# Optimization experiments

Measured on AMD Instinct MI355X. Metric: run time of the kernel, lower is better.

The kernel has to match this reference:

```python
import jax, jax.numpy as jnp
import numpy as np

B, T, D = 2, 2048, 2048
H, HD = 16, 128
ROPE_BASE = 10000.0
EPS = 1e-6


def setup_inputs() -> dict:
    key = jax.random.key(0)
    ks = jax.random.split(key, 5)
    s = 1.0 / np.sqrt(D)
    return {
        "x": jax.random.normal(ks[0], (B, T, D), dtype=jnp.float32),
        "Wq": jax.random.normal(ks[1], (H * HD, D), dtype=jnp.float32) * s,
        "Wk": jax.random.normal(ks[2], (H * HD, D), dtype=jnp.float32) * s,
        "Wv": jax.random.normal(ks[3], (H * HD, D), dtype=jnp.float32) * s,
        "Wo": jax.random.normal(ks[4], (D, H * HD), dtype=jnp.float32) * s,
        "q_norm_w": jnp.ones((HD,), dtype=jnp.float32),
        "k_norm_w": jnp.ones((HD,), dtype=jnp.float32),
    }


def _rms_norm(x, w):
    # RMSNorm over last dim, no centering (LLaMA/Qwen style)
    norm = jnp.sqrt(jnp.mean(jnp.square(x), axis=-1, keepdims=True) + EPS)
    return x / norm * w


def _rope_interleaved(x):
    # x: (B, T, H, HD); GPT-NeoX interleaved style, sequential positions
    dim = HD // 2
    freqs = jnp.exp(-jnp.arange(0, dim, dtype=jnp.float32) * jnp.log(ROPE_BASE) / dim)
    angles = jnp.arange(T, dtype=jnp.float32)[:, None] * freqs[None, :]  # (T, dim)
    cos = jnp.cos(angles)[None, :, None, :]  # (1, T, 1, dim)
    sin = jnp.sin(angles)[None, :, None, :]
    x_even = x[..., ::2]
    x_odd = x[..., 1::2]
    r_even = x_even * cos - x_odd * sin
    r_odd = x_even * sin + x_odd * cos
    return jnp.stack([r_even, r_odd], axis=-1).reshape(x.shape)


def reference(x, Wq, Wk, Wv, Wo, q_norm_w, k_norm_w):
    # QKV projections (weights stored [out, in], per llm_linear einsum)
    q = jnp.einsum("btd,od->bto", x, Wq).reshape(B, T, H, HD)
    k = jnp.einsum("btd,od->bto", x, Wk).reshape(B, T, H, HD)
    v = jnp.einsum("btd,od->bto", x, Wv).reshape(B, T, H, HD)
    # per-head QK RMSNorm
    q = _rms_norm(q, q_norm_w)
    k = _rms_norm(k, k_norm_w)
    # rotary embeddings
    q = _rope_interleaved(q)
    k = _rope_interleaved(k)
    # causal scaled dot-product attention
    scale = 1.0 / jnp.sqrt(jnp.asarray(HD, dtype=x.dtype))
    scores = jnp.einsum("bthd,bshd->bhts", q, k) * scale  # (B, H, T, T)
    causal = jnp.tril(jnp.ones((T, T), dtype=bool))
    scores = jnp.where(causal[None, None, :, :], scores, jnp.asarray(-1e30, dtype=scores.dtype))
    probs = jax.nn.softmax(scores, axis=-1)
    ctx = jnp.einsum("bhts,bshd->bthd", probs, v).reshape(B, T, H * HD)
    # output projection
    return jnp.einsum("bto,do->btd", ctx, Wo)
```

## Files before the change

### kernel.cpp

```cpp
#include <hip/hip_runtime.h>
#include <cstdint>
#include <cstddef>

#define B_ 2
#define T_ 2048
#define D_ 2048
#define H_ 16
#define HD_ 128
#define EPS_ 1e-6f
#define QSCALE_ 0.08838834764831845f
#define KVSTRIDE_ (H_ * HD_)

typedef unsigned short u16;
typedef short s16x8 __attribute__((ext_vector_type(8)));
typedef float f32x4 __attribute__((ext_vector_type(4)));

__device__ __forceinline__ float bf2f(u16 h) {
  union { unsigned int u; float f; } v;
  v.u = ((unsigned int)h) << 16;
  return v.f;
}
__device__ __forceinline__ u16 f2bf(float f) {
  union { float f; unsigned int u; } v;
  v.f = f;
  unsigned int r = v.u + 0x7FFFu + ((v.u >> 16) & 1u);
  return (u16)(r >> 16);
}

__device__ __forceinline__ void gload16(const void* g, void* l) {
  __builtin_amdgcn_global_load_lds(
      (const __attribute__((address_space(1))) unsigned int*)g,
      (__attribute__((address_space(3))) unsigned int*)l, 16, 0, 0);
}

__global__ void cvt_f32_bf16(const float* __restrict__ in, u16* __restrict__ out, int n4) {
  int i = blockIdx.x * blockDim.x + threadIdx.x;
  if (i < n4) {
    float4 v = ((const float4*)in)[i];
    ((ushort4*)out)[i] = make_ushort4(f2bf(v.x), f2bf(v.y), f2bf(v.z), f2bf(v.w));
  }
}

template <int OUT_BF16>
__global__ __launch_bounds__(256, 2) void gemm_btn(const u16* __restrict__ A,
                                                   const u16* __restrict__ Bm,
                                                   void* __restrict__ Cout,
                                                   int M, int N, int K) {
  __shared__ u16 As[2 * 128 * 32];
  __shared__ u16 Bs[2 * 128 * 32];
  const int tid = threadIdx.x;
  const int w = tid >> 6, lane = tid & 63, quad = lane >> 4, c = lane & 15;
  const int wm = w & 1, wn = w >> 1;
  const int m0 = blockIdx.y * 128, n0 = blockIdx.x * 128;

  f32x4 acc[4][4];
#pragma unroll
  for (int i = 0; i < 4; ++i)
#pragma unroll
    for (int j = 0; j < 4; ++j) acc[i][j] = (f32x4){0.f, 0.f, 0.f, 0.f};

  for (int k0 = 0; k0 < K; k0 += 64) {
    __syncthreads();
#pragma unroll
    for (int i = 0; i < 4; ++i) {
      int chunk = (w * 4 + i) * 64 + lane;
      int kc = chunk >> 9;
      int within = chunk & 511;
      int row = within >> 2, cc = within & 3;
      gload16(A + (size_t)(m0 + row) * K + k0 + kc * 32 + cc * 8, (void*)(As + chunk * 8));
      gload16(Bm + (size_t)(n0 + row) * K + k0 + kc * 32 + cc * 8, (void*)(Bs + chunk * 8));
    }
    __syncthreads();
#pragma unroll
    for (int kc = 0; kc < 2; ++kc) {
      s16x8 af[4], bf[4];
#pragma unroll
      for (int mi = 0; mi < 4; ++mi)
        af[mi] = *(const s16x8*)(As + kc * 4096 + (wm * 64 + mi * 16 + c) * 32 + quad * 8);
#pragma unroll
      for (int ni = 0; ni < 4; ++ni)
        bf[ni] = *(const s16x8*)(Bs + kc * 4096 + (wn * 64 + ni * 16 + c) * 32 + quad * 8);
#pragma unroll
      for (int mi = 0; mi < 4; ++mi)
#pragma unroll
        for (int ni = 0; ni < 4; ++ni)
          acc[mi][ni] = __builtin_amdgcn_mfma_f32_16x16x32_bf16(af[mi], bf[ni], acc[mi][ni], 0, 0, 0);
    }
  }

#pragma unroll
  for (int mi = 0; mi < 4; ++mi)
#pragma unroll
    for (int ni = 0; ni < 4; ++ni)
#pragma unroll
      for (int r = 0; r < 4; ++r) {
        int row = m0 + wm * 64 + mi * 16 + quad * 4 + r;
        int col = n0 + wn * 64 + ni * 16 + c;
        float v = acc[mi][ni][r];
        if (OUT_BF16)
          ((u16*)Cout)[(size_t)row * N + col] = f2bf(v);
        else
          ((float*)Cout)[(size_t)row * N + col] = v;
      }
}

__global__ void rmsnorm_rope(u16* __restrict__ x, const float* __restrict__ nw, float outscale) {
  const int tid = threadIdx.x;
  const int w = tid >> 6, lane = tid & 63;
  const int vec = blockIdx.x * 4 + w;
  const int t = (vec >> 4) & (T_ - 1);
  u16* base = x + (size_t)vec * HD_;
  unsigned int pk = *(const unsigned int*)(base + lane * 2);
  float e = bf2f((u16)(pk & 0xFFFFu));
  float o = bf2f((u16)(pk >> 16));
  float ss = e * e + o * o;
#pragma unroll
  for (int off = 1; off < 64; off <<= 1) ss += __shfl_xor(ss, off, 64);
  float rn = rsqrtf(ss * (1.0f / HD_) + EPS_);
  float we = nw[lane * 2], wo = nw[lane * 2 + 1];
  e = e * rn * we;
  o = o * rn * wo;
  float freq = expf(-(float)lane * (9.210340371976184f / 64.0f));
  float ang = (float)t * freq;
  float sn, cs;
  sincosf(ang, &sn, &cs);
  float re = (e * cs - o * sn) * outscale;
  float ro = (e * sn + o * cs) * outscale;
  *(unsigned int*)(base + lane * 2) = ((unsigned int)f2bf(ro) << 16) | (unsigned int)f2bf(re);
}

__global__ __launch_bounds__(256, 2) void attn_fwd(const u16* __restrict__ Q,
                                                   const u16* __restrict__ Kg,
                                                   const u16* __restrict__ Vt,
                                                   u16* __restrict__ O) {
  __shared__ u16 Ks[64 * 136];
  __shared__ u16 Vts[128 * 72];
  __shared__ u16 Ps[64 * 72];
  const int tid = threadIdx.x;
  const int w = tid >> 6, lane = tid & 63, quad = lane >> 4, c = lane & 15;
  const int bid = blockIdx.x;
  const int qt = 31 - (bid >> 5);
  const int h = bid & 15;
  const int b = (bid >> 4) & 1;
  const int q0 = qt * 64;

  s16x8 qf[4];
  const u16* qbase = Q + ((size_t)(b * T_ + q0 + w * 16 + c) * H_ + h) * HD_;
#pragma unroll
  for (int kk = 0; kk < 4; ++kk) qf[kk] = *(const s16x8*)(qbase + kk * 32 + quad * 8);

  f32x4 of[8];
#pragma unroll
  for (int i = 0; i < 8; ++i) of[i] = (f32x4){0.f, 0.f, 0.f, 0.f};
  float m_i[4] = {-1e30f, -1e30f, -1e30f, -1e30f};
  float l_i[4] = {0.f, 0.f, 0.f, 0.f};

  const u16* kbase = Kg + ((size_t)b * T_ * H_ + h) * HD_;
  const u16* vtbase = Vt + (size_t)(h * HD_) * (B_ * T_) + (size_t)b * T_;

  for (int j = 0; j <= qt; ++j) {
    __syncthreads();
    const u16* krow = kbase + (size_t)(j * 64) * KVSTRIDE_;
    const u16* vrow = vtbase + j * 64;
#pragma unroll
    for (int i = 0; i < 4; ++i) {
      int chunk = i * 256 + tid;
      int krowi = chunk >> 4, kc = chunk & 15;
      *(uint4*)(&Ks[krowi * 136 + kc * 8]) =
          *(const uint4*)(krow + (size_t)krowi * KVSTRIDE_ + kc * 8);
      int vrowi = chunk >> 3, vc = chunk & 7;
      *(uint4*)(&Vts[vrowi * 72 + vc * 8]) =
          *(const uint4*)(vrow + (size_t)vrowi * (B_ * T_) + vc * 8);
    }
    __syncthreads();

    f32x4 sf[4];
#pragma unroll
    for (int ni = 0; ni < 4; ++ni) {
      f32x4 a = (f32x4){0.f, 0.f, 0.f, 0.f};
#pragma unroll
      for (int kk = 0; kk < 4; ++kk) {
        s16x8 bfr = *(const s16x8*)(&Ks[(ni * 16 + c) * 136 + kk * 32 + quad * 8]);
        a = __builtin_amdgcn_mfma_f32_16x16x32_bf16(qf[kk], bfr, a, 0, 0, 0);
      }
      sf[ni] = a;
    }
    if (j == qt) {
#pragma unroll
      for (int ni = 0; ni < 4; ++ni)
#pragma unroll
        for (int r = 0; r < 4; ++r) {
          int rowg = w * 16 + quad * 4 + r;
          int colg = ni * 16 + c;
          if (colg > rowg) sf[ni][r] = -1e30f;
        }
    }
    float mc[4];
#pragma unroll
    for (int r = 0; r < 4; ++r)
      mc[r] = fmaxf(fmaxf(sf[0][r], sf[1][r]), fmaxf(sf[2][r], sf[3][r]));
#pragma unroll
    for (int off = 1; off < 16; off <<= 1)
#pragma unroll
      for (int r = 0; r < 4; ++r) mc[r] = fmaxf(mc[r], __shfl_xor(mc[r], off, 64));
#pragma unroll
    for (int r = 0; r < 4; ++r) {
      float mnew = fmaxf(m_i[r], mc[r]);
      float alpha = __expf(m_i[r] - mnew);
      m_i[r] = mnew;
      l_i[r] *= alpha;
#pragma unroll
      for (int ot = 0; ot < 8; ++ot) of[ot][r] *= alpha;
    }
    float rs[4] = {0.f, 0.f, 0.f, 0.f};
#pragma unroll
    for (int ni = 0; ni < 4; ++ni)
#pragma unroll
      for (int r = 0; r < 4; ++r) {
        float p = __expf(sf[ni][r] - m_i[r]);
        sf[ni][r] = p;
        rs[r] += p;
      }
#pragma unroll
    for (int off = 1; off < 16; off <<= 1)
#pragma unroll
      for (int r = 0; r < 4; ++r) rs[r] += __shfl_xor(rs[r], off, 64);
#pragma unroll
    for (int r = 0; r < 4; ++r) l_i[r] += rs[r];
#pragma unroll
    for (int ni = 0; ni < 4; ++ni)
#pragma unroll
      for (int r = 0; r < 4; ++r)
        Ps[(w * 16 + quad * 4 + r) * 72 + ni * 16 + c] = f2bf(sf[ni][r]);
    __syncthreads();
    s16x8 pa[2];
    pa[0] = *(const s16x8*)(&Ps[(w * 16 + c) * 72 + quad * 8]);
    pa[1] = *(const s16x8*)(&Ps[(w * 16 + c) * 72 + 32 + quad * 8]);
#pragma unroll
    for (int ot = 0; ot < 8; ++ot) {
#pragma unroll
      for (int kk = 0; kk < 2; ++kk) {
        s16x8 vfr = *(const s16x8*)(&Vts[(ot * 16 + c) * 72 + kk * 32 + quad * 8]);
        of[ot] = __builtin_amdgcn_mfma_f32_16x16x32_bf16(pa[kk], vfr, of[ot], 0, 0, 0);
      }
    }
  }

  float inv[4];
#pragma unroll
  for (int r = 0; r < 4; ++r) inv[r] = 1.0f / l_i[r];
  u16* obase = O + ((size_t)(b * T_ + q0) * H_ + h) * HD_;
#pragma unroll
  for (int ot = 0; ot < 8; ++ot)
#pragma unroll
    for (int r = 0; r < 4; ++r)
      obase[(size_t)(w * 16 + quad * 4 + r) * KVSTRIDE_ + ot * 16 + c] = f2bf(of[ot][r] * inv[r]);
}

extern "C" void kernel_launch(void* const* d_in, const int* in_sizes, int n_in,
                              void* d_out, int out_size, void* d_ws, size_t ws_size,
                              hipStream_t stream) {
  const float* x = (const float*)d_in[0];
  const float* Wq = (const float*)d_in[1];
  const float* Wk = (const float*)d_in[2];
  const float* Wv = (const float*)d_in[3];
  const float* Wo = (const float*)d_in[4];
  const float* qw = (const float*)d_in[5];
  const float* kw = (const float*)d_in[6];
  float* out = (float*)d_out;

  const size_t xE = (size_t)B_ * T_ * D_;
  const size_t wE = (size_t)D_ * H_ * HD_;
  const size_t need = xE * 2 * 5 + wE * 2 * 4;
  if (ws_size < need) return;

  char* ws = (char*)d_ws;
  u16* xb = (u16*)ws;   ws += xE * 2;
  u16* wqb = (u16*)ws;  ws += wE * 2;
  u16* wkb = (u16*)ws;  ws += wE * 2;
  u16* wvb = (u16*)ws;  ws += wE * 2;
  u16* wob = (u16*)ws;  ws += wE * 2;
  u16* qb = (u16*)ws;   ws += xE * 2;
  u16* kb = (u16*)ws;   ws += xE * 2;
  u16* vtb = (u16*)ws;  ws += xE * 2;
  u16* ctxb = (u16*)ws; ws += xE * 2;

  cvt_f32_bf16<<<xE / 1024, 256, 0, stream>>>(x, xb, (int)(xE / 4));
  cvt_f32_bf16<<<wE / 1024, 256, 0, stream>>>(Wq, wqb, (int)(wE / 4));
  cvt_f32_bf16<<<wE / 1024, 256, 0, stream>>>(Wk, wkb, (int)(wE / 4));
  cvt_f32_bf16<<<wE / 1024, 256, 0, stream>>>(Wv, wvb, (int)(wE / 4));
  cvt_f32_bf16<<<wE / 1024, 256, 0, stream>>>(Wo, wob, (int)(wE / 4));

  dim3 gg(16, 32);
  gemm_btn<1><<<gg, 256, 0, stream>>>(xb, wqb, qb, 4096, 2048, 2048);
  gemm_btn<1><<<gg, 256, 0, stream>>>(xb, wkb, kb, 4096, 2048, 2048);
  dim3 ggv(32, 16);
  gemm_btn<1><<<ggv, 256, 0, stream>>>(wvb, xb, vtb, 2048, 4096, 2048);

  rmsnorm_rope<<<16384, 256, 0, stream>>>(qb, qw, QSCALE_);
  rmsnorm_rope<<<16384, 256, 0, stream>>>(kb, kw, 1.0f);

  attn_fwd<<<B_ * H_ * (T_ / 64), 256, 0, stream>>>(qb, kb, vtb, ctxb);

  gemm_btn<0><<<gg, 256, 0, stream>>>(ctxb, wob, out, 4096, 2048, 2048);
}
```

Measured before the change: 420.2 us.

## Double attention query tile to 128 rows, reusing each K/V tile twice

The attention kernel now has each block process 128 query rows instead of 64, with each wave owning two 16-row MFMA sub-tiles. Each K and V tile staged in shared memory is therefore used by twice as many rows, which halves global K/V traffic and load/sync overhead per unit of work. The block-wide barrier between writing P to shared memory and reading it back is dropped, since each wave only reads its own rows. In exchange, register pressure roughly doubles for accumulators (risking spills under launch_bounds(256,2)), the grid halves to 512 blocks, and causal load imbalance gets coarser.

```diff
diff --git a/kernel.cpp b/kernel.cpp
--- a/kernel.cpp
+++ b/kernel.cpp
@@ -135,30 +135,39 @@
                                                    u16* __restrict__ O) {
   __shared__ u16 Ks[64 * 136];
   __shared__ u16 Vts[128 * 72];
-  __shared__ u16 Ps[64 * 72];
+  __shared__ u16 Ps[128 * 72];
   const int tid = threadIdx.x;
   const int w = tid >> 6, lane = tid & 63, quad = lane >> 4, c = lane & 15;
   const int bid = blockIdx.x;
-  const int qt = 31 - (bid >> 5);
+  const int qt = 15 - (bid >> 5);
   const int h = bid & 15;
   const int b = (bid >> 4) & 1;
-  const int q0 = qt * 64;
-
-  s16x8 qf[4];
-  const u16* qbase = Q + ((size_t)(b * T_ + q0 + w * 16 + c) * H_ + h) * HD_;
-#pragma unroll
-  for (int kk = 0; kk < 4; ++kk) qf[kk] = *(const s16x8*)(qbase + kk * 32 + quad * 8);
-
-  f32x4 of[8];
-#pragma unroll
-  for (int i = 0; i < 8; ++i) of[i] = (f32x4){0.f, 0.f, 0.f, 0.f};
-  float m_i[4] = {-1e30f, -1e30f, -1e30f, -1e30f};
-  float l_i[4] = {0.f, 0.f, 0.f, 0.f};
+  const int q0 = qt * 128;
+  const int jmax = 2 * qt + 1;
+
+  s16x8 qf[2][4];
+#pragma unroll
+  for (int mi = 0; mi < 2; ++mi) {
+    const u16* qbase = Q + ((size_t)(b * T_ + q0 + w * 32 + mi * 16 + c) * H_ + h) * HD_;
+#pragma unroll
+    for (int kk = 0; kk < 4; ++kk) qf[mi][kk] = *(const s16x8*)(qbase + kk * 32 + quad * 8);
+  }
+
+  f32x4 of[2][8];
+#pragma unroll
+  for (int mi = 0; mi < 2; ++mi)
+#pragma unroll
+    for (int ot = 0; ot < 8; ++ot) of[mi][ot] = (f32x4){0.f, 0.f, 0.f, 0.f};
+  float m_i[2][4], l_i[2][4];
+#pragma unroll
+  for (int mi = 0; mi < 2; ++mi)
+#pragma unroll
+    for (int r = 0; r < 4; ++r) { m_i[mi][r] = -1e30f; l_i[mi][r] = 0.f; }
 
   const u16* kbase = Kg + ((size_t)b * T_ * H_ + h) * HD_;
   const u16* vtbase = Vt + (size_t)(h * HD_) * (B_ * T_) + (size_t)b * T_;
 
-  for (int j = 0; j <= qt; ++j) {
+  for (int j = 0; j <= jmax; ++j) {
     __syncthreads();
     const u16* krow = kbase + (size_t)(j * 64) * KVSTRIDE_;
     const u16* vrow = vtbase + j * 64;
@@ -174,87 +183,107 @@
     }
     __syncthreads();
 
-    f32x4 sf[4];
+    f32x4 sf[2][4];
 #pragma unroll
     for (int ni = 0; ni < 4; ++ni) {
-      f32x4 a = (f32x4){0.f, 0.f, 0.f, 0.f};
-#pragma unroll
-      for (int kk = 0; kk < 4; ++kk) {
-        s16x8 bfr = *(const s16x8*)(&Ks[(ni * 16 + c) * 136 + kk * 32 + quad * 8]);
-        a = __builtin_amdgcn_mfma_f32_16x16x32_bf16(qf[kk], bfr, a, 0, 0, 0);
+      s16x8 kf[4];
+#pragma unroll
+      for (int kk = 0; kk < 4; ++kk)
+        kf[kk] = *(const s16x8*)(&Ks[(ni * 16 + c) * 136 + kk * 32 + quad * 8]);
+#pragma unroll
+      for (int mi = 0; mi < 2; ++mi) {
+        f32x4 a = (f32x4){0.f, 0.f, 0.f, 0.f};
+#pragma unroll
+        for (int kk = 0; kk < 4; ++kk)
+          a = __builtin_amdgcn_mfma_f32_16x16x32_bf16(qf[mi][kk], kf[kk], a, 0, 0, 0);
+        sf[mi][ni] = a;
       }
-      sf[ni] = a;
-    }
-    if (j == qt) {
+    }
+    if (j >= 2 * qt) {
+#pragma unroll
+      for (int mi = 0; mi < 2; ++mi)
+#pragma unroll
+        for (int ni = 0; ni < 4; ++ni)
+#pragma unroll
+          for (int r = 0; r < 4; ++r) {
+            int rowg = q0 + w * 32 + mi * 16 + quad * 4 + r;
+            int colg = j * 64 + ni * 16 + c;
+            if (colg > rowg) sf[mi][ni][r] = -1e30f;
+          }
+    }
+#pragma unroll
+    for (int mi = 0; mi < 2; ++mi) {
+      float mc[4];
+#pragma unroll
+      for (int r = 0; r < 4; ++r)
+        mc[r] = fmaxf(fmaxf(sf[mi][0][r], sf[mi][1][r]), fmaxf(sf[mi][2][r], sf[mi][3][r]));
+#pragma unroll
+      for (int off = 1; off < 16; off <<= 1)
+#pragma unroll
+        for (int r = 0; r < 4; ++r) mc[r] = fmaxf(mc[r], __shfl_xor(mc[r], off, 64));
+#pragma unroll
+      for (int r = 0; r < 4; ++r) {
+        float mnew = fmaxf(m_i[mi][r], mc[r]);
+        float alpha = __expf(m_i[mi][r] - mnew);
+        m_i[mi][r] = mnew;
+        l_i[mi][r] *= alpha;
+#pragma unroll
+        for (int ot = 0; ot < 8; ++ot) of[mi][ot][r] *= alpha;
+      }
+      float rs[4] = {0.f, 0.f, 0.f, 0.f};
 #pragma unroll
       for (int ni = 0; ni < 4; ++ni)
 #pragma unroll
         for (int r = 0; r < 4; ++r) {
-          int rowg = w * 16 + quad * 4 + r;
-          int colg = ni * 16 + c;
-          if (colg > rowg) sf[ni][r] = -1e30f;
+          float p = __expf(sf[mi][ni][r] - m_i[mi][r]);
+          sf[mi][ni][r] = p;
+          rs[r] += p;
         }
-    }
-    float mc[4];
-#pragma unroll
-    for (int r = 0; r < 4; ++r)
-      mc[r] = fmaxf(fmaxf(sf[0][r], sf[1][r]), fmaxf(sf[2][r], sf[3][r]));
-#pragma unroll
-    for (int off = 1; off < 16; off <<= 1)
-#pragma unroll
-      for (int r = 0; r < 4; ++r) mc[r] = fmaxf(mc[r], __shfl_xor(mc[r], off, 64));
-#pragma unroll
-    for (int r = 0; r < 4; ++r) {
-      float mnew = fmaxf(m_i[r], mc[r]);
-      float alpha = __expf(m_i[r] - mnew);
-      m_i[r] = mnew;
-      l_i[r] *= alpha;
-#pragma unroll
-      for (int ot = 0; ot < 8; ++ot) of[ot][r] *= alpha;
-    }
-    float rs[4] = {0.f, 0.f, 0.f, 0.f};
-#pragma unroll
-    for (int ni = 0; ni < 4; ++ni)
-#pragma unroll
-      for (int r = 0; r < 4; ++r) {
-        float p = __expf(sf[ni][r] - m_i[r]);
-        sf[ni][r] = p;
-        rs[r] += p;
-      }
-#pragma unroll
-    for (int off = 1; off < 16; off <<= 1)
-#pragma unroll
-      for (int r = 0; r < 4; ++r) rs[r] += __shfl_xor(rs[r], off, 64);
-#pragma unroll
-    for (int r = 0; r < 4; ++r) l_i[r] += rs[r];
-#pragma unroll
-    for (int ni = 0; ni < 4; ++ni)
+#pragma unroll
+      for (int off = 1; off < 16; off <<= 1)
+#pragma unroll
+        for (int r = 0; r < 4; ++r) rs[r] += __shfl_xor(rs[r], off, 64);
+#pragma unroll
+      for (int r = 0; r < 4; ++r) l_i[mi][r] += rs[r];
+#pragma unroll
+      for (int ni = 0; ni < 4; ++ni)
+#pragma unroll
+        for (int r = 0; r < 4; ++r)
+          Ps[(w * 32 + mi * 16 + quad * 4 + r) * 72 + ni * 16 + c] = f2bf(sf[mi][ni][r]);
+    }
+    s16x8 pa[2][2];
+#pragma unroll
+    for (int mi = 0; mi < 2; ++mi)
+#pragma unroll
+      for (int kk = 0; kk < 2; ++kk)
+        pa[mi][kk] = *(const s16x8*)(&Ps[(w * 32 + mi * 16 + c) * 72 + kk * 32 + quad * 8]);
+#pragma unroll
+    for (int ot = 0; ot < 8; ++ot) {
+      s16x8 vf[2];
+#pragma unroll
+      for (int kk = 0; kk < 2; ++kk)
+        vf[kk] = *(const s16x8*)(&Vts[(ot * 16 + c) * 72 + kk * 32 + quad * 8]);
+#pragma unroll
+      for (int mi = 0; mi < 2; ++mi)
+#pragma unroll
+        for (int kk = 0; kk < 2; ++kk)
+          of[mi][ot] = __builtin_amdgcn_mfma_f32_16x16x32_bf16(pa[mi][kk], vf[kk], of[mi][ot], 0, 0, 0);
+    }
+  }
+
+  u16* obase = O + ((size_t)(b * T_ + q0 + w * 32) * H_ + h) * HD_;
+#pragma unroll
+  for (int mi = 0; mi < 2; ++mi) {
+    float inv[4];
+#pragma unroll
+    for (int r = 0; r < 4; ++r) inv[r] = 1.0f / l_i[mi][r];
+#pragma unroll
+    for (int ot = 0; ot < 8; ++ot)
 #pragma unroll
       for (int r = 0; r < 4; ++r)
-        Ps[(w * 16 + quad * 4 + r) * 72 + ni * 16 + c] = f2bf(sf[ni][r]);
-    __syncthreads();
-    s16x8 pa[2];
-    pa[0] = *(const s16x8*)(&Ps[(w * 16 + c) * 72 + quad * 8]);
-    pa[1] = *(const s16x8*)(&Ps[(w * 16 + c) * 72 + 32 + quad * 8]);
-#pragma unroll
-    for (int ot = 0; ot < 8; ++ot) {
-#pragma unroll
-      for (int kk = 0; kk < 2; ++kk) {
-        s16x8 vfr = *(const s16x8*)(&Vts[(ot * 16 + c) * 72 + kk * 32 + quad * 8]);
-        of[ot] = __builtin_amdgcn_mfma_f32_16x16x32_bf16(pa[kk], vfr, of[ot], 0, 0, 0);
-      }
-    }
-  }
-
-  float inv[4];
-#pragma unroll
-  for (int r = 0; r < 4; ++r) inv[r] = 1.0f / l_i[r];
-  u16* obase = O + ((size_t)(b * T_ + q0) * H_ + h) * HD_;
-#pragma unroll
-  for (int ot = 0; ot < 8; ++ot)
-#pragma unroll
-    for (int r = 0; r < 4; ++r)
-      obase[(size_t)(w * 16 + quad * 4 + r) * KVSTRIDE_ + ot * 16 + c] = f2bf(of[ot][r] * inv[r]);
+        obase[(size_t)(mi * 16 + quad * 4 + r) * KVSTRIDE_ + ot * 16 + c] =
+            f2bf(of[mi][ot][r] * inv[r]);
+  }
 }
 
 extern "C" void kernel_launch(void* const* d_in, const int* in_sizes, int n_in,
@@ -300,7 +329,7 @@
   rmsnorm_rope<<<16384, 256, 0, stream>>>(qb, qw, QSCALE_);
   rmsnorm_rope<<<16384, 256, 0, stream>>>(kb, kw, 1.0f);
 
-  attn_fwd<<<B_ * H_ * (T_ / 64), 256, 0, stream>>>(qb, kb, vtb, ctxb);
+  attn_fwd<<<B_ * H_ * (T_ / 128), 256, 0, stream>>>(qb, kb, vtb, ctxb);
 
   gemm_btn<0><<<gg, 256, 0, stream>>>(ctxb, wob, out, 4096, 2048, 2048);
 }
```

After: 435.0 us. 1.04x slower.
